# Kernel tuning notes

Measured on AMD Instinct MI355X. Metric: run time of the kernel, lower is better.

The kernel has to match this reference:

```python
import jax, jax.numpy as jnp
import numpy as np

B, C, H, W = 8, 256, 224, 224
OUT = 256
NUM_LEVELS = 3
LN_EPS = 1e-5


def _grid_pool(x, g):
    # deterministic grid max-pool: output is (B, C, g, g)
    b, c, h, w = x.shape
    ph, pw = (-h) % g, (-w) % g
    if ph or pw:
        x = jnp.pad(x, ((0, 0), (0, 0), (0, ph), (0, pw)), mode='reflect')
    kh, kw = (h + ph) // g, (w + pw) // g
    return x.reshape(b, c, g, kh, g, kw).max(axis=(3, 5))


def _get_coords(batch, g, dtype):
    # normalized (cx, cy, w, h) per grid cell -> (batch, g*g, 4)
    centers = (jnp.arange(g, dtype=dtype) + 0.5) / g
    gy, gx = jnp.meshgrid(centers, centers, indexing='ij')
    cxy = jnp.stack([gx, gy], axis=-1).reshape(-1, 2)
    wh = jnp.full((g * g, 2), 1.0 / g, dtype=dtype)
    bboxes = jnp.concatenate([cxy, wh], axis=-1)
    return jnp.broadcast_to(bboxes[None], (batch, g * g, 4))


def setup_inputs() -> dict:
    key = jax.random.key(0)
    kx, kw = jax.random.split(key, 2)
    x = jax.random.normal(kx, (B, C, H, W), dtype=jnp.float32)
    # threshold_init = 0.5 -> logit = 0
    logit_thresholds = jnp.zeros((NUM_LEVELS,), jnp.float32)
    ln_gamma = jnp.ones((C,), jnp.float32)
    ln_beta = jnp.zeros((C,), jnp.float32)
    # torch Linear weight is (out, in); stored here as (in, out)
    w_proj = jax.random.normal(kw, (C, OUT), jnp.float32) / np.float32(np.sqrt(C))
    b_proj = jnp.zeros((OUT,), jnp.float32)
    return dict(x=x, logit_thresholds=logit_thresholds, ln_gamma=ln_gamma,
                ln_beta=ln_beta, w_proj=w_proj, b_proj=b_proj)


def reference(x, logit_thresholds, ln_gamma, ln_beta, w_proj, b_proj):
    dtype = x.dtype
    coarse_g = 2 ** (NUM_LEVELS - 1)  # 4
    coarse = _grid_pool(x, coarse_g)  # (B, C, 4, 4)
    coords = _get_coords(B, coarse_g, dtype)  # (B, 16, 4)

    # importance: L2 norm over channels of coarse cells (aggregate=False,
    # contrast-norm skipped since coarse_level == num_levels-1)
    feat_flat = coarse.reshape(B, C, -1).transpose(0, 2, 1)  # (B, 16, C)
    importance = jnp.sqrt(jnp.sum(feat_flat * feat_flat, axis=-1))  # (B, 16)
    imp_min = importance.min(axis=1, keepdims=True)
    imp_max = importance.max(axis=1, keepdims=True)
    imp01 = (importance - imp_min) / (imp_max - imp_min + 1e-8)

    thresh = jax.nn.sigmoid(logit_thresholds)[NUM_LEVELS - 1]
    bg_hard = (imp01 >= thresh).astype(dtype)
    bg_soft = jax.nn.sigmoid((imp01 - thresh) * 10.0)
    # straight-through estimator
    bg_mask = bg_hard - jax.lax.stop_gradient(bg_soft) + bg_soft
    mask = jnp.maximum(bg_mask, jnp.zeros((), dtype))  # hard_target == 0 (no target_mask)

    # fill_mode='upsample': bilinear (align_corners=False == half-pixel) 4x4 -> HxW
    mask_2d = mask.reshape(B, coarse_g, coarse_g)
    final_soft_mask = jax.image.resize(mask_2d, (B, H, W), method='bilinear')

    # training path: multiply by soft mask
    out_sparse = x * final_soft_mask[:, None, :, :]

    # proj = LayerNorm + Linear over all coarse cells; keep via hard mask
    mu = feat_flat.mean(axis=-1, keepdims=True)
    var = feat_flat.var(axis=-1, keepdims=True)
    normed = (feat_flat - mu) * jax.lax.rsqrt(var + LN_EPS) * ln_gamma + ln_beta
    proj = jnp.einsum('bnc,co->bno', normed, w_proj) + b_proj  # (B, 16, OUT)
    keep = (mask > 0.5).astype(dtype)  # (B, 16)
    kept_feats = proj * keep[..., None]
    kept_coords = coords * keep[..., None]
    return out_sparse, kept_feats, kept_coords, keep
```

## Files before the change

kernel.cpp:

```cpp
#include <hip/hip_runtime.h>

#define BB 8
#define CC 256
#define HH 224
#define WW 224
#define OUTC 256
#define PLANE (HH*WW)
#define LN_EPS 1e-5f

#define OFF_FEATS  102760448
#define OFF_COORDS 102793216
#define OFF_KEEP   102793728

#define WS_COARSE 0
#define WS_MU     32768
#define WS_RSTD   32896
#define WS_KEEP   33024
#define WS_MX     33152

#define NV8 (BB*CC*HH*WW/8)

__global__ __launch_bounds__(448) void pool_kernel(const float* __restrict__ x,
                                                   float* __restrict__ coarse) {
    int blk = blockIdx.x;
    int gy  = blk & 3;
    int bc  = blk >> 2;
    int t   = threadIdx.x;
    int chunk = t % 56;
    int rowg  = t / 56;
    int gx    = chunk / 14;

    const float* p = x + (size_t)bc * PLANE + (size_t)(gy * 56) * WW + chunk * 4;
    float m = -INFINITY;
#pragma unroll
    for (int it = 0; it < 7; ++it) {
        float4 v = *(const float4*)(p + (size_t)(it * 8 + rowg) * WW);
        m = fmaxf(m, fmaxf(fmaxf(v.x, v.y), fmaxf(v.z, v.w)));
    }
    __shared__ float red[512];
    red[gx * 128 + rowg * 14 + (chunk % 14)] = m;
    if (t < 64) red[(t / 16) * 128 + 112 + (t % 16)] = -INFINITY;
    __syncthreads();
    if (t < 256) {
        int w = t >> 6, lane = t & 63;
        float v = fmaxf(red[w * 128 + lane], red[w * 128 + 64 + lane]);
        for (int s = 32; s; s >>= 1) v = fmaxf(v, __shfl_down(v, s, 64));
        if (lane == 0) {
            int b = bc >> 8, c = bc & 255;
            coarse[(b * 16 + gy * 4 + w) * 256 + c] = v;
        }
    }
}

__global__ __launch_bounds__(256) void stats_kernel(const float* __restrict__ coarse,
                                                    const float* __restrict__ logit_th,
                                                    float* __restrict__ keep_out,
                                                    float* __restrict__ coords_out,
                                                    float* __restrict__ muv,
                                                    float* __restrict__ rstdv,
                                                    float* __restrict__ keepf,
                                                    float* __restrict__ mx) {
    int b = blockIdx.x;
    int t = threadIdx.x;
    int wave = t >> 6, lane = t & 63;
    __shared__ float ssum[16 * 8], ssq[16 * 8];
    __shared__ float simp[16], smask[16];
    const float* cb = coarse + b * 4096;

    for (int n = 0; n < 16; ++n) {
        float f = cb[n * 256 + t];
        float s = f, q = f * f;
        for (int d = 32; d; d >>= 1) {
            s += __shfl_down(s, d, 64);
            q += __shfl_down(q, d, 64);
        }
        if (lane == 0) { ssum[n * 8 + wave] = s; ssq[n * 8 + wave] = q; }
    }
    __syncthreads();
    if (t < 16) {
        int n = t;
        float s = ssum[n * 8] + ssum[n * 8 + 1] + ssum[n * 8 + 2] + ssum[n * 8 + 3];
        float q = ssq[n * 8] + ssq[n * 8 + 1] + ssq[n * 8 + 2] + ssq[n * 8 + 3];
        simp[n] = sqrtf(q);
        float mu  = s * (1.0f / 256.0f);
        float var = q * (1.0f / 256.0f) - mu * mu;
        muv[b * 16 + n]   = mu;
        rstdv[b * 16 + n] = rsqrtf(var + LN_EPS);
    }
    __syncthreads();
    if (t < 16) {
        int n = t;
        float mn = simp[0], mxv = simp[0];
        for (int k = 1; k < 16; ++k) { mn = fminf(mn, simp[k]); mxv = fmaxf(mxv, simp[k]); }
        float imp01 = (simp[n] - mn) / (mxv - mn + 1e-8f);
        float lt = logit_th[2];
        float th = 1.0f / (1.0f + expf(-lt));
        float hard = (imp01 >= th) ? 1.0f : 0.0f;
        float soft = 1.0f / (1.0f + expf(-10.0f * (imp01 - th)));
        float mv = fmaxf((hard - soft) + soft, 0.0f);
        float kp = (mv > 0.5f) ? 1.0f : 0.0f;
        smask[n] = mv;
        keepf[b * 16 + n] = kp;
        keep_out[b * 16 + n] = kp;
        int gy = n >> 2, gx = n & 3;
        float cx = (gx + 0.5f) * 0.25f;
        float cy = (gy + 0.5f) * 0.25f;
        float* co = coords_out + (b * 16 + n) * 4;
        co[0] = cx * kp;
        co[1] = cy * kp;
        co[2] = 0.25f * kp;
        co[3] = 0.25f * kp;
    }
    __syncthreads();
    for (int k = t; k < 4 * WW; k += 256) {
        int p = k / WW, j = k % WW;
        float u = (j + 0.5f) * (1.0f / 56.0f) - 0.5f;
        float x0f = floorf(u);
        float fx = u - x0f;
        int x0 = (int)x0f;
        int x0c = min(max(x0, 0), 3);
        int x1c = min(x0 + 1, 3);
        float a = smask[p * 4 + x0c];
        float bq = smask[p * 4 + x1c];
        mx[(b * 4 + p) * WW + j] = a + fx * (bq - a);
    }
}

__global__ __launch_bounds__(256) void proj_kernel(const float* __restrict__ coarse,
                                                   const float* __restrict__ gamma,
                                                   const float* __restrict__ beta,
                                                   const float* __restrict__ wp,
                                                   const float* __restrict__ bp,
                                                   const float* __restrict__ muv,
                                                   const float* __restrict__ rstdv,
                                                   const float* __restrict__ keepf,
                                                   float* __restrict__ feats_out) {
    int bn = blockIdx.x;
    int t  = threadIdx.x;
    __shared__ float sn[256];
    float mu = muv[bn], rs = rstdv[bn], kp = keepf[bn];
    float f  = coarse[bn * 256 + t];
    float nv = (f - mu) * rs;
    nv = nv * gamma[t] + beta[t];
    sn[t] = nv;
    __syncthreads();
    float acc = 0.0f;
#pragma unroll 4
    for (int c = 0; c < 256; ++c) {
        acc += sn[c] * wp[c * 256 + t];
    }
    feats_out[bn * 256 + t] = (acc + bp[t]) * kp;
}

__global__ __launch_bounds__(256) void sparse_kernel(const float* __restrict__ x,
                                                     const float* __restrict__ mx,
                                                     float* __restrict__ out) {
    int gid0 = blockIdx.x * 256 + threadIdx.x;
    int gid  = (NV8 - 1) - gid0;
    int j8  = gid % 28;
    int rem = gid / 28;
    int i   = rem % HH;
    int bc  = rem / HH;
    int b   = bc >> 8;

    float u   = (i + 0.5f) * (1.0f / 56.0f) - 0.5f;
    float y0f = floorf(u);
    float fy  = u - y0f;
    int y0  = (int)y0f;
    int y0c = min(max(y0, 0), 3);
    int y1c = min(y0 + 1, 3);

    const float* r0 = mx + (b * 4 + y0c) * WW + j8 * 8;
    const float* r1 = mx + (b * 4 + y1c) * WW + j8 * 8;
    float4 a0 = *(const float4*)(r0);
    float4 a1 = *(const float4*)(r0 + 4);
    float4 b0 = *(const float4*)(r1);
    float4 b1 = *(const float4*)(r1 + 4);

    float m0 = a0.x + fy * (b0.x - a0.x);
    float m1 = a0.y + fy * (b0.y - a0.y);
    float m2 = a0.z + fy * (b0.z - a0.z);
    float m3 = a0.w + fy * (b0.w - a0.w);
    float m4 = a1.x + fy * (b1.x - a1.x);
    float m5 = a1.y + fy * (b1.y - a1.y);
    float m6 = a1.z + fy * (b1.z - a1.z);
    float m7 = a1.w + fy * (b1.w - a1.w);

    size_t off = (size_t)gid * 8;
    bool nz = (m0 != 0.0f) | (m1 != 0.0f) | (m2 != 0.0f) | (m3 != 0.0f) |
              (m4 != 0.0f) | (m5 != 0.0f) | (m6 != 0.0f) | (m7 != 0.0f);
    if (!nz) {
        *(float4*)(out + off)     = make_float4(0.f, 0.f, 0.f, 0.f);
        *(float4*)(out + off + 4) = make_float4(0.f, 0.f, 0.f, 0.f);
        return;
    }
    float4 x0 = *(const float4*)(x + off);
    float4 x1 = *(const float4*)(x + off + 4);
    float4 o0 = make_float4(x0.x * m0, x0.y * m1, x0.z * m2, x0.w * m3);
    float4 o1 = make_float4(x1.x * m4, x1.y * m5, x1.z * m6, x1.w * m7);
    *(float4*)(out + off)     = o0;
    *(float4*)(out + off + 4) = o1;
}

extern "C" void kernel_launch(void* const* d_in, const int* in_sizes, int n_in,
                              void* d_out, int out_size, void* d_ws, size_t ws_size,
                              hipStream_t stream) {
    const float* x     = (const float*)d_in[0];
    const float* lt    = (const float*)d_in[1];
    const float* gamma = (const float*)d_in[2];
    const float* beta  = (const float*)d_in[3];
    const float* wp    = (const float*)d_in[4];
    const float* bp    = (const float*)d_in[5];
    float* out = (float*)d_out;
    float* ws  = (float*)d_ws;

    float* coarse = ws + WS_COARSE;
    float* muv    = ws + WS_MU;
    float* rstdv  = ws + WS_RSTD;
    float* keepf  = ws + WS_KEEP;
    float* mx     = ws + WS_MX;

    pool_kernel<<<BB * CC * 4, 448, 0, stream>>>(x, coarse);
    stats_kernel<<<BB, 256, 0, stream>>>(coarse, lt, out + OFF_KEEP, out + OFF_COORDS,
                                         muv, rstdv, keepf, mx);
    proj_kernel<<<BB * 16, 256, 0, stream>>>(coarse, gamma, beta, wp, bp,
                                             muv, rstdv, keepf, out + OFF_FEATS);
    sparse_kernel<<<NV8 / 256, 256, 0, stream>>>(x, mx, out);
}
```

Before: 765.0 us.

## Fuse stats and projection kernels; use nontemporal loads/stores in sparse pass

Merges the per-batch stats kernel and the per-cell projection kernel into one kernel. Each of the 8 blocks now normalizes all 16 cells into shared memory and computes the 16 projections with a register accumulator array, which removes one launch and the workspace round-trip. The sparse masking kernel switches to nontemporal vector loads and stores so the large streaming traffic bypasses cache retention. The fused projection runs on only 8 blocks instead of 128, so its parallelism is much lower and it may take longer.

```diff
diff --git a/kernel.cpp b/kernel.cpp
--- a/kernel.cpp
+++ b/kernel.cpp
@@ -13,12 +13,11 @@
 #define OFF_KEEP   102793728
 
 #define WS_COARSE 0
-#define WS_MU     32768
-#define WS_RSTD   32896
-#define WS_KEEP   33024
 #define WS_MX     33152
 
 #define NV8 (BB*CC*HH*WW/8)
+
+typedef float vf4 __attribute__((ext_vector_type(4)));
 
 __global__ __launch_bounds__(448) void pool_kernel(const float* __restrict__ x,
                                                    float* __restrict__ coarse) {
@@ -52,19 +51,23 @@
     }
 }
 
-__global__ __launch_bounds__(256) void stats_kernel(const float* __restrict__ coarse,
-                                                    const float* __restrict__ logit_th,
-                                                    float* __restrict__ keep_out,
-                                                    float* __restrict__ coords_out,
-                                                    float* __restrict__ muv,
-                                                    float* __restrict__ rstdv,
-                                                    float* __restrict__ keepf,
-                                                    float* __restrict__ mx) {
+__global__ __launch_bounds__(256) void stats_proj_kernel(
+        const float* __restrict__ coarse,
+        const float* __restrict__ logit_th,
+        const float* __restrict__ gamma,
+        const float* __restrict__ beta,
+        const float* __restrict__ wp,
+        const float* __restrict__ bp,
+        float* __restrict__ keep_out,
+        float* __restrict__ coords_out,
+        float* __restrict__ feats_out,
+        float* __restrict__ mx) {
     int b = blockIdx.x;
     int t = threadIdx.x;
     int wave = t >> 6, lane = t & 63;
-    __shared__ float ssum[16 * 8], ssq[16 * 8];
-    __shared__ float simp[16], smask[16];
+    __shared__ float ssum[16 * 4], ssq[16 * 4];
+    __shared__ float simp[16], smask[16], skeep[16], smu[16], srstd[16];
+    __shared__ float sn[16][256];
     const float* cb = coarse + b * 4096;
 
     for (int n = 0; n < 16; ++n) {
@@ -74,18 +77,18 @@
             s += __shfl_down(s, d, 64);
             q += __shfl_down(q, d, 64);
         }
-        if (lane == 0) { ssum[n * 8 + wave] = s; ssq[n * 8 + wave] = q; }
+        if (lane == 0) { ssum[n * 4 + wave] = s; ssq[n * 4 + wave] = q; }
     }
     __syncthreads();
     if (t < 16) {
         int n = t;
-        float s = ssum[n * 8] + ssum[n * 8 + 1] + ssum[n * 8 + 2] + ssum[n * 8 + 3];
-        float q = ssq[n * 8] + ssq[n * 8 + 1] + ssq[n * 8 + 2] + ssq[n * 8 + 3];
+        float s = ssum[n * 4] + ssum[n * 4 + 1] + ssum[n * 4 + 2] + ssum[n * 4 + 3];
+        float q = ssq[n * 4] + ssq[n * 4 + 1] + ssq[n * 4 + 2] + ssq[n * 4 + 3];
         simp[n] = sqrtf(q);
         float mu  = s * (1.0f / 256.0f);
         float var = q * (1.0f / 256.0f) - mu * mu;
-        muv[b * 16 + n]   = mu;
-        rstdv[b * 16 + n] = rsqrtf(var + LN_EPS);
+        smu[n]   = mu;
+        srstd[n] = rsqrtf(var + LN_EPS);
     }
     __syncthreads();
     if (t < 16) {
@@ -100,7 +103,7 @@
         float mv = fmaxf((hard - soft) + soft, 0.0f);
         float kp = (mv > 0.5f) ? 1.0f : 0.0f;
         smask[n] = mv;
-        keepf[b * 16 + n] = kp;
+        skeep[n] = kp;
         keep_out[b * 16 + n] = kp;
         int gy = n >> 2, gx = n & 3;
         float cx = (gx + 0.5f) * 0.25f;
@@ -124,32 +127,24 @@
         float bq = smask[p * 4 + x1c];
         mx[(b * 4 + p) * WW + j] = a + fx * (bq - a);
     }
-}
-
-__global__ __launch_bounds__(256) void proj_kernel(const float* __restrict__ coarse,
-                                                   const float* __restrict__ gamma,
-                                                   const float* __restrict__ beta,
-                                                   const float* __restrict__ wp,
-                                                   const float* __restrict__ bp,
-                                                   const float* __restrict__ muv,
-                                                   const float* __restrict__ rstdv,
-                                                   const float* __restrict__ keepf,
-                                                   float* __restrict__ feats_out) {
-    int bn = blockIdx.x;
-    int t  = threadIdx.x;
-    __shared__ float sn[256];
-    float mu = muv[bn], rs = rstdv[bn], kp = keepf[bn];
-    float f  = coarse[bn * 256 + t];
-    float nv = (f - mu) * rs;
-    nv = nv * gamma[t] + beta[t];
-    sn[t] = nv;
-    __syncthreads();
-    float acc = 0.0f;
-#pragma unroll 4
+    for (int n = 0; n < 16; ++n) {
+        float f = cb[n * 256 + t];
+        float nv = (f - smu[n]) * srstd[n];
+        sn[n][t] = nv * gamma[t] + beta[t];
+    }
+    __syncthreads();
+    float acc[16];
+#pragma unroll
+    for (int n = 0; n < 16; ++n) acc[n] = 0.0f;
     for (int c = 0; c < 256; ++c) {
-        acc += sn[c] * wp[c * 256 + t];
-    }
-    feats_out[bn * 256 + t] = (acc + bp[t]) * kp;
+        float wv = wp[c * 256 + t];
+#pragma unroll
+        for (int n = 0; n < 16; ++n) acc[n] += sn[n][c] * wv;
+    }
+    float bb = bp[t];
+#pragma unroll
+    for (int n = 0; n < 16; ++n)
+        feats_out[(b * 16 + n) * 256 + t] = (acc[n] + bb) * skeep[n];
 }
 
 __global__ __launch_bounds__(256) void sparse_kernel(const float* __restrict__ x,
@@ -172,10 +167,10 @@
 
     const float* r0 = mx + (b * 4 + y0c) * WW + j8 * 8;
     const float* r1 = mx + (b * 4 + y1c) * WW + j8 * 8;
-    float4 a0 = *(const float4*)(r0);
-    float4 a1 = *(const float4*)(r0 + 4);
-    float4 b0 = *(const float4*)(r1);
-    float4 b1 = *(const float4*)(r1 + 4);
+    vf4 a0 = *(const vf4*)(r0);
+    vf4 a1 = *(const vf4*)(r0 + 4);
+    vf4 b0 = *(const vf4*)(r1);
+    vf4 b1 = *(const vf4*)(r1 + 4);
 
     float m0 = a0.x + fy * (b0.x - a0.x);
     float m1 = a0.y + fy * (b0.y - a0.y);
@@ -190,16 +185,17 @@
     bool nz = (m0 != 0.0f) | (m1 != 0.0f) | (m2 != 0.0f) | (m3 != 0.0f) |
               (m4 != 0.0f) | (m5 != 0.0f) | (m6 != 0.0f) | (m7 != 0.0f);
     if (!nz) {
-        *(float4*)(out + off)     = make_float4(0.f, 0.f, 0.f, 0.f);
-        *(float4*)(out + off + 4) = make_float4(0.f, 0.f, 0.f, 0.f);
+        vf4 z = 0.0f;
+        __builtin_nontemporal_store(z, (vf4*)(out + off));
+        __builtin_nontemporal_store(z, (vf4*)(out + off + 4));
         return;
     }
-    float4 x0 = *(const float4*)(x + off);
-    float4 x1 = *(const float4*)(x + off + 4);
-    float4 o0 = make_float4(x0.x * m0, x0.y * m1, x0.z * m2, x0.w * m3);
-    float4 o1 = make_float4(x1.x * m4, x1.y * m5, x1.z * m6, x1.w * m7);
-    *(float4*)(out + off)     = o0;
-    *(float4*)(out + off + 4) = o1;
+    vf4 x0 = __builtin_nontemporal_load((const vf4*)(x + off));
+    vf4 x1 = __builtin_nontemporal_load((const vf4*)(x + off + 4));
+    vf4 o0; o0.x = x0.x * m0; o0.y = x0.y * m1; o0.z = x0.z * m2; o0.w = x0.w * m3;
+    vf4 o1; o1.x = x1.x * m4; o1.y = x1.y * m5; o1.z = x1.z * m6; o1.w = x1.w * m7;
+    __builtin_nontemporal_store(o0, (vf4*)(out + off));
+    __builtin_nontemporal_store(o1, (vf4*)(out + off + 4));
 }
 
 extern "C" void kernel_launch(void* const* d_in, const int* in_sizes, int n_in,
@@ -215,15 +211,11 @@
     float* ws  = (float*)d_ws;
 
     float* coarse = ws + WS_COARSE;
-    float* muv    = ws + WS_MU;
-    float* rstdv  = ws + WS_RSTD;
-    float* keepf  = ws + WS_KEEP;
     float* mx     = ws + WS_MX;
 
     pool_kernel<<<BB * CC * 4, 448, 0, stream>>>(x, coarse);
-    stats_kernel<<<BB, 256, 0, stream>>>(coarse, lt, out + OFF_KEEP, out + OFF_COORDS,
-                                         muv, rstdv, keepf, mx);
-    proj_kernel<<<BB * 16, 256, 0, stream>>>(coarse, gamma, beta, wp, bp,
-                                             muv, rstdv, keepf, out + OFF_FEATS);
+    stats_proj_kernel<<<BB, 256, 0, stream>>>(coarse, lt, gamma, beta, wp, bp,
+                                              out + OFF_KEEP, out + OFF_COORDS,
+                                              out + OFF_FEATS, mx);
     sparse_kernel<<<NV8 / 256, 256, 0, stream>>>(x, mx, out);
 }
```

Measured after the change: 753.4 us. Within noise of the previous version (-1.5%).
